# Optimization experiments

Measured on AMD Instinct MI355X. Metric: run time of the kernel, lower is better.

Reference implementation:

```python
import jax, jax.numpy as jnp
import numpy as np

B, L, D, H = 2, 2048, 2048, 16
Dh = D // H
THETA = 10000.0
NEG = -1e9


def _rope_tables(length, offset=0):
    # inv_freq: [Dh/2], positions: [L]
    inv_freq = 1.0 / (THETA ** (jnp.arange(0, Dh, 2, dtype=jnp.float32) / Dh))
    pos = jnp.arange(offset, offset + length, dtype=jnp.float32)
    freqs = pos[:, None] * inv_freq[None, :]           # [L, Dh/2]
    emb = jnp.concatenate([freqs, freqs], axis=-1)     # [L, Dh]
    return jnp.cos(emb), jnp.sin(emb)


def _rotate_half(t):
    t1, t2 = t[..., : Dh // 2], t[..., Dh // 2:]
    return jnp.concatenate([-t2, t1], axis=-1)


def setup_inputs() -> dict:
    key = jax.random.key(0)
    k1, k2, k3 = jax.random.split(key, 3)
    x = jax.random.normal(k1, (B, L, D), dtype=jnp.float32)
    attention_mask = jnp.ones((B, L), dtype=jnp.int32)
    w_qkv = jax.random.normal(k2, (D, 3 * D), dtype=jnp.float32) * (D ** -0.5)
    w_proj = jax.random.normal(k3, (D, D), dtype=jnp.float32) * (D ** -0.5)
    return {"x": x, "attention_mask": attention_mask, "w_qkv": w_qkv, "w_proj": w_proj}


def reference(x, attention_mask, w_qkv, w_proj):
    # QKV projection (no bias)
    qkv = x @ w_qkv                                    # [B, L, 3D]
    q, k, v = jnp.split(qkv, 3, axis=-1)
    q = q.reshape(B, L, H, Dh).transpose(0, 2, 1, 3)   # [B, H, L, Dh]
    k = k.reshape(B, L, H, Dh).transpose(0, 2, 1, 3)
    v = v.reshape(B, L, H, Dh).transpose(0, 2, 1, 3)

    # RoPE (past_len = 0)
    cos, sin = _rope_tables(L)                         # [L, Dh]
    q = q * cos + _rotate_half(q) * sin
    k = k * cos + _rotate_half(k) * sin

    # causal + key-padding mask (True = masked out)
    causal = jnp.triu(jnp.ones((L, L), dtype=bool), k=1)         # [L, L]
    pad = (attention_mask == 0)[:, None, None, :]                # [B,1,1,L]
    mask = causal[None, None, :, :] | pad                        # [B,1,L,L]

    scale = Dh ** -0.5
    scores = jnp.einsum("bhqd,bhkd->bhqk", q, k) * scale         # [B,H,L,L]
    scores = jnp.where(mask, NEG, scores)
    attn = jax.nn.softmax(scores, axis=-1)
    y = jnp.einsum("bhqk,bhkd->bhqd", attn, v)                   # [B,H,L,Dh]
    y = y.transpose(0, 2, 1, 3).reshape(B, L, D)
    return y @ w_proj
```

## Files before the change

### kernel.cpp

```cpp
#include <hip/hip_runtime.h>
#include <hip/hip_bf16.h>

typedef unsigned short ushort_t;
typedef __attribute__((ext_vector_type(4))) float fvec4;
typedef __attribute__((ext_vector_type(16))) float fvec16;
typedef __attribute__((ext_vector_type(8))) short short8;
typedef __attribute__((ext_vector_type(4))) unsigned short usvec4;
typedef __attribute__((ext_vector_type(2))) unsigned int uvec2;

typedef const __attribute__((address_space(1))) void* gas_ptr;
typedef __attribute__((address_space(3))) void* las_ptr;

__device__ __forceinline__ void glds16(const void* g, void* l) {
  __builtin_amdgcn_global_load_lds((gas_ptr)g, (las_ptr)l, 16, 0, 0);
}

__device__ __forceinline__ ushort_t f2bf(float f) {
  unsigned u = __float_as_uint(f);
  u += 0x7FFFu + ((u >> 16) & 1u);
  return (ushort_t)(u >> 16);
}
__device__ __forceinline__ float bf2f(ushort_t h) {
  return __uint_as_float(((unsigned)h) << 16);
}

__device__ __forceinline__ void swap32(unsigned& a, unsigned& b) {
#if __has_builtin(__builtin_amdgcn_permlane32_swap)
  uvec2 r = __builtin_amdgcn_permlane32_swap(a, b, false, false);
  a = r[0]; b = r[1];
#else
  const unsigned sa = (unsigned)__shfl_xor((int)a, 32);
  const unsigned sb = (unsigned)__shfl_xor((int)b, 32);
  const bool hi = (threadIdx.x & 32) != 0;
  const unsigned na = hi ? sb : a;
  const unsigned nb = hi ? b : sa;
  a = na; b = nb;
#endif
}

__global__ __launch_bounds__(256) void cast_f32_bf16(const float* __restrict__ X,
                                                     ushort_t* __restrict__ Xb) {
  const size_t i = ((size_t)blockIdx.x * 256 + threadIdx.x) * 4;
  const fvec4 v = *(const fvec4*)(X + i);
  usvec4 o;
  o[0] = f2bf(v[0]); o[1] = f2bf(v[1]); o[2] = f2bf(v[2]); o[3] = f2bf(v[3]);
  *(usvec4*)(Xb + i) = o;
}

__global__ __launch_bounds__(256) void tcast(const float* __restrict__ W,
                                             ushort_t* __restrict__ Wt,
                                             const int Kd, const int Nd) {
  __shared__ float ls[64][65];
  const int t = threadIdx.x;
  const int n0 = blockIdx.x * 64, k0 = blockIdx.y * 64;
  const int kr = t >> 4, nc = (t & 15) * 4;
#pragma unroll
  for (int it = 0; it < 4; ++it) {
    const fvec4 v = *(const fvec4*)(W + (size_t)(k0 + it * 16 + kr) * Nd + n0 + nc);
    ls[it * 16 + kr][nc + 0] = v[0];
    ls[it * 16 + kr][nc + 1] = v[1];
    ls[it * 16 + kr][nc + 2] = v[2];
    ls[it * 16 + kr][nc + 3] = v[3];
  }
  __syncthreads();
  const int nr = t >> 2, kg = (t & 3) * 16;
  __align__(16) ushort_t tmp[16];
#pragma unroll
  for (int i = 0; i < 16; ++i) tmp[i] = f2bf(ls[kg + i][nr]);
  ushort_t* dst = Wt + (size_t)(n0 + nr) * Kd + k0 + kg;
  *(short8*)(dst)     = *(const short8*)(tmp);
  *(short8*)(dst + 8) = *(const short8*)(tmp + 8);
}

#define FENCE asm volatile("" ::: "memory")

__device__ __forceinline__ void stage_one(const ushort_t* __restrict__ G, const int grow,
                                          const int K, const int tk, ushort_t* ldsmat,
                                          const int lrow0, const int wv, const int lane) {
  const int rr = lane >> 3;
  const int kk = ((lane & 7) ^ rr) * 8;
  glds16(G + (size_t)(grow + wv * 8 + rr) * K + tk + kk,
         ldsmat + (lrow0 + wv * 8) * 64);
}

__device__ __forceinline__ short8 frag_ld(const ushort_t* ldsmat, const int rbase,
                                          const int kc, const int quad, const int mm) {
  const int r = rbase + mm;
  const int blk = r >> 6;
  const int pblk = ((blk & 1) << 1) | (blk >> 1);
  const int ldsrow = pblk * 64 + (r & 63);
  const int kb = (kc * 64 + quad * 16) ^ ((mm & 7) << 4);
  return *(const short8*)(ldsmat + ldsrow * 64 + (kb >> 1));
}

__device__ __forceinline__ short8 fragld128(const ushort_t* mat, const int row,
                                            const int kc, const int quad) {
  const int kb = (kc * 64 + quad * 16) ^ ((row & 7) << 4);
  return *(const short8*)(mat + row * 64 + (kb >> 1));
}

#define G192_LDA(Am, q_)                                                      \
  short8 af[2][2];                                                            \
  af[0][0] = frag_ld(Am, wr * 128 + (q_) * 32,      0, quad, mm);             \
  af[0][1] = frag_ld(Am, wr * 128 + (q_) * 32,      1, quad, mm);             \
  af[1][0] = frag_ld(Am, wr * 128 + (q_) * 32 + 16, 0, quad, mm);             \
  af[1][1] = frag_ld(Am, wr * 128 + (q_) * 32 + 16, 1, quad, mm);

#define G192_LDB(Bm)                                                          \
  _Pragma("unroll")                                                           \
  for (int j = 0; j < 3; ++j) {                                               \
    bfr[j][0] = fragld128(Bm, wc * 48 + j * 16 + mm, 0, quad);                \
    bfr[j][1] = fragld128(Bm, wc * 48 + j * 16 + mm, 1, quad);                \
  }

#define G192_MFMA(q_)                                                         \
  __builtin_amdgcn_s_setprio(1);                                              \
  _Pragma("unroll")                                                           \
  for (int ii = 0; ii < 2; ++ii)                                              \
  _Pragma("unroll")                                                           \
  for (int j = 0; j < 3; ++j) {                                               \
    acc[(q_) * 2 + ii][j] = __builtin_amdgcn_mfma_f32_16x16x32_bf16(          \
        af[ii][0], bfr[j][0], acc[(q_) * 2 + ii][j], 0, 0, 0);                \
    acc[(q_) * 2 + ii][j] = __builtin_amdgcn_mfma_f32_16x16x32_bf16(          \
        af[ii][1], bfr[j][1], acc[(q_) * 2 + ii][j], 0, 0, 0);                \
  }                                                                           \
  __builtin_amdgcn_s_setprio(0);

__global__ __launch_bounds__(512, 2) void gemm192(
    const ushort_t* __restrict__ A, const ushort_t* __restrict__ Bt,
    const int M, const int N, const int K, const int mode,
    float* __restrict__ C,
    ushort_t* __restrict__ Qo, ushort_t* __restrict__ Ko, ushort_t* __restrict__ Vo) {
  __shared__ __align__(16) ushort_t lds[2][28672];

  const int tid = threadIdx.x, wv = tid >> 6, lane = tid & 63;
  const int quad = lane >> 4, mm = lane & 15;
  const int wr = wv >> 2, wc = wv & 3;

  const int nwg = gridDim.x, ntx = N / 192;
  const int bid = blockIdx.x;
  const int swz = (bid & 7) * (nwg >> 3) + (bid >> 3);
  const int by = swz / ntx, bx = swz - by * ntx;
  const int row0 = by * 256, col0 = bx * 192;

  fvec4 acc[8][3];
#pragma unroll
  for (int i = 0; i < 8; ++i)
#pragma unroll
    for (int j = 0; j < 3; ++j) acc[i][j] = (fvec4){0.f, 0.f, 0.f, 0.f};

  short8 bfr[3][2];

  ushort_t* A0 = &lds[0][0];      ushort_t* B0 = &lds[0][16384];
  ushort_t* A1 = &lds[1][0];      ushort_t* B1 = &lds[1][16384];

  stage_one(Bt, col0 + 0,   K, 0,  B0, 0,   wv, lane); FENCE;
  stage_one(Bt, col0 + 64,  K, 0,  B0, 64,  wv, lane); FENCE;
  stage_one(Bt, col0 + 128, K, 0,  B0, 128, wv, lane); FENCE;
  stage_one(A,  row0 + 0,   K, 0,  A0, 0,   wv, lane); FENCE;
  stage_one(A,  row0 + 64,  K, 0,  A0, 128, wv, lane); FENCE;
  stage_one(A,  row0 + 128, K, 0,  A0, 64,  wv, lane); FENCE;
  stage_one(A,  row0 + 192, K, 0,  A0, 192, wv, lane); FENCE;
  stage_one(Bt, col0 + 0,   K, 64, B1, 0,   wv, lane); FENCE;
  stage_one(Bt, col0 + 64,  K, 64, B1, 64,  wv, lane); FENCE;
  stage_one(Bt, col0 + 128, K, 64, B1, 128, wv, lane); FENCE;
  stage_one(A,  row0 + 0,   K, 64, A1, 0,   wv, lane); FENCE;
  stage_one(A,  row0 + 128, K, 64, A1, 64,  wv, lane); FENCE;
  asm volatile("s_waitcnt vmcnt(5)" ::: "memory");
  __builtin_amdgcn_s_barrier();

  const int nit = K >> 7;
  for (int i = 0; i < nit; ++i) {
    const bool more = (i + 1 < nit);
    const int kA = i * 128 + 64;
    const int kB = i * 128 + 128;
    const int kC = i * 128 + 192;
    {
      __builtin_amdgcn_s_barrier();
      G192_LDA(A0, 0);
      G192_LDB(B0);
      stage_one(A, row0 + 64,  K, kA, A1, 128, wv, lane); FENCE;
      stage_one(A, row0 + 192, K, kA, A1, 192, wv, lane);
      G192_MFMA(0);
    }
    {
      __builtin_amdgcn_s_barrier();
      G192_LDA(A0, 1);
      if (more) { stage_one(Bt, col0 + 0,  K, kB, B0, 0,  wv, lane); FENCE;
                  stage_one(Bt, col0 + 64, K, kB, B0, 64, wv, lane); }
      G192_MFMA(1);
    }
    {
      __builtin_amdgcn_s_barrier();
      G192_LDA(A0, 2);
      if (more) stage_one(Bt, col0 + 128, K, kB, B0, 128, wv, lane);
      G192_MFMA(2);
    }
    {
      __builtin_amdgcn_s_barrier();
      G192_LDA(A0, 3);
      if (more) {
        stage_one(A, row0 + 0,   K, kB, A0, 0,  wv, lane); FENCE;
        stage_one(A, row0 + 128, K, kB, A0, 64, wv, lane);
        asm volatile("s_waitcnt vmcnt(5)" ::: "memory");
      } else {
        asm volatile("s_waitcnt vmcnt(0)" ::: "memory");
      }
      G192_MFMA(3);
    }
    {
      __builtin_amdgcn_s_barrier();
      G192_LDA(A1, 0);
      G192_LDB(B1);
      if (more) { stage_one(A, row0 + 64,  K, kB, A0, 128, wv, lane); FENCE;
                  stage_one(A, row0 + 192, K, kB, A0, 192, wv, lane); }
      G192_MFMA(0);
    }
    {
      __builtin_amdgcn_s_barrier();
      G192_LDA(A1, 1);
      if (more) { stage_one(Bt, col0 + 0,  K, kC, B1, 0,  wv, lane); FENCE;
                  stage_one(Bt, col0 + 64, K, kC, B1, 64, wv, lane); }
      G192_MFMA(1);
    }
    {
      __builtin_amdgcn_s_barrier();
      G192_LDA(A1, 2);
      if (more) stage_one(Bt, col0 + 128, K, kC, B1, 128, wv, lane);
      G192_MFMA(2);
    }
    {
      __builtin_amdgcn_s_barrier();
      G192_LDA(A1, 3);
      if (more) {
        stage_one(A, row0 + 0,   K, kC, A1, 0,  wv, lane); FENCE;
        stage_one(A, row0 + 128, K, kC, A1, 64, wv, lane);
        asm volatile("s_waitcnt vmcnt(5)" ::: "memory");
      }
      G192_MFMA(3);
    }
  }

  if (mode == 0) {
#pragma unroll
    for (int i = 0; i < 8; ++i)
#pragma unroll
      for (int r = 0; r < 4; ++r) {
        const int row = row0 + wr * 128 + i * 16 + quad * 4 + r;
        float* cr = C + (size_t)row * N + col0 + wc * 48;
#pragma unroll
        for (int j = 0; j < 3; ++j) cr[j * 16 + mm] = acc[i][j][r];
      }
  } else {
#pragma unroll
    for (int j = 0; j < 3; ++j) {
      const int gcolj = col0 + wc * 48 + j * 16;
      const int which = gcolj >> 11;
      const int h = (gcolj >> 7) & 15;
      const int coff = (gcolj & 127) + mm;
      ushort_t* dst = (which == 0) ? Qo : (which == 1) ? Ko : Vo;
#pragma unroll
      for (int i = 0; i < 8; ++i)
#pragma unroll
        for (int r = 0; r < 4; ++r) {
          const int row = row0 + wr * 128 + i * 16 + quad * 4 + r;
          const int bb = row >> 11, l = row & 2047;
          dst[((size_t)(bb * 16 + h) * 2048 + l) * 128 + coff] = f2bf(acc[i][j][r]);
        }
    }
  }
}

__device__ __forceinline__ void stage_a128(const ushort_t* __restrict__ G, const int row0,
                                           const int K, const int tk, ushort_t* ldsA,
                                           const int wv, const int lane) {
  const int rr = lane >> 3;
  const int kk = ((lane & 7) ^ rr) * 8;
  const int r = wv * 8 + rr;
  glds16(G + (size_t)(row0 + r) * K + tk + kk,      ldsA + (wv * 8) * 64);
  glds16(G + (size_t)(row0 + 64 + r) * K + tk + kk, ldsA + (64 + wv * 8) * 64);
}
__device__ __forceinline__ void stage_b128(const ushort_t* __restrict__ G, const int col0,
                                           const int K, const int tk, ushort_t* ldsB,
                                           const int u, const int wv, const int lane) {
  const int rr = lane >> 3;
  const int kk = ((lane & 7) ^ rr) * 8;
  const int r = u * 64 + wv * 8 + rr;
  glds16(G + (size_t)(col0 + r) * K + tk + kk,       ldsB + (u * 64 + wv * 8) * 64);
  glds16(G + (size_t)(col0 + 128 + r) * K + tk + kk, ldsB + (128 + u * 64 + wv * 8) * 64);
}

__global__ __launch_bounds__(512, 2) void gemm128(
    const ushort_t* __restrict__ A, const ushort_t* __restrict__ Bt,
    const int M, const int N, const int K, const int mode,
    float* __restrict__ C,
    ushort_t* __restrict__ Qo, ushort_t* __restrict__ Ko, ushort_t* __restrict__ Vo) {
  __shared__ __align__(16) ushort_t l128[2][24576];

  const int tid = threadIdx.x, wv = tid >> 6, lane = tid & 63;
  const int quad = lane >> 4, mm = lane & 15;
  const int wr = wv >> 2, wc = wv & 3;

  const int nwg = gridDim.x, ntx = N >> 8;
  const int bid = blockIdx.x;
  const int swz = (bid & 7) * (nwg >> 3) + (bid >> 3);
  const int by = swz / ntx, bx = swz - by * ntx;
  const int row0 = by * 128, col0 = bx * 256;

  fvec4 acc[4][4];
#pragma unroll
  for (int m = 0; m < 4; ++m)
#pragma unroll
    for (int j = 0; j < 4; ++j) acc[m][j] = (fvec4){0.f, 0.f, 0.f, 0.f};

  ushort_t* A0 = &l128[0][0];     ushort_t* B0 = &l128[0][8192];
  ushort_t* A1 = &l128[1][0];     ushort_t* B1 = &l128[1][8192];

  short8 bfr[4][2];

  stage_b128(Bt, col0, K, 0,  B0, 0, wv, lane); FENCE;
  stage_b128(Bt, col0, K, 0,  B0, 1, wv, lane); FENCE;
  stage_a128(A,  row0, K, 0,  A0,    wv, lane); FENCE;
  stage_b128(Bt, col0, K, 64, B1, 0, wv, lane); FENCE;
  stage_b128(Bt, col0, K, 64, B1, 1, wv, lane); FENCE;
  asm volatile("s_waitcnt vmcnt(4)" ::: "memory");
  __builtin_amdgcn_s_barrier();

  const int nit = K >> 7;
  for (int i = 0; i < nit; ++i) {
    const bool more = (i + 1 < nit);
    const int kA = i * 128 + 64;
    const int kB = i * 128 + 128;
    const int kC = i * 128 + 192;
    {
      stage_a128(A, row0, K, kA, A1, wv, lane);
      short8 af[4];
#pragma unroll
      for (int m = 0; m < 4; ++m) af[m] = fragld128(A0, wr * 64 + m * 16 + mm, 0, quad);
#pragma unroll
      for (int j = 0; j < 4; ++j) {
        bfr[j][0] = fragld128(B0, wc * 64 + j * 16 + mm, 0, quad);
        bfr[j][1] = fragld128(B0, wc * 64 + j * 16 + mm, 1, quad);
      }
      __builtin_amdgcn_s_setprio(1);
#pragma unroll
      for (int m = 0; m < 4; ++m)
#pragma unroll
        for (int j = 0; j < 4; ++j)
          acc[m][j] = __builtin_amdgcn_mfma_f32_16x16x32_bf16(af[m], bfr[j][0], acc[m][j], 0, 0, 0);
      __builtin_amdgcn_s_setprio(0);
      asm volatile("s_waitcnt lgkmcnt(0)" ::: "memory");
      __builtin_amdgcn_sched_barrier(0);
    }
    {
      __builtin_amdgcn_s_barrier();
      if (more) { stage_b128(Bt, col0, K, kB, B0, 0, wv, lane); FENCE;
                  stage_b128(Bt, col0, K, kB, B0, 1, wv, lane); FENCE; }
      if (more) { asm volatile("s_waitcnt vmcnt(4)" ::: "memory"); }
      else      { asm volatile("s_waitcnt vmcnt(0)" ::: "memory"); }
      short8 af[4];
#pragma unroll
      for (int m = 0; m < 4; ++m) af[m] = fragld128(A0, wr * 64 + m * 16 + mm, 1, quad);
      __builtin_amdgcn_s_setprio(1);
#pragma unroll
      for (int m = 0; m < 4; ++m)
#pragma unroll
        for (int j = 0; j < 4; ++j)
          acc[m][j] = __builtin_amdgcn_mfma_f32_16x16x32_bf16(af[m], bfr[j][1], acc[m][j], 0, 0, 0);
      __builtin_amdgcn_s_setprio(0);
    }
    {
      __builtin_amdgcn_s_barrier();
      if (more) stage_a128(A, row0, K, kB, A0, wv, lane);
      short8 af[4];
#pragma unroll
      for (int m = 0; m < 4; ++m) af[m] = fragld128(A1, wr * 64 + m * 16 + mm, 0, quad);
#pragma unroll
      for (int j = 0; j < 4; ++j) {
        bfr[j][0] = fragld128(B1, wc * 64 + j * 16 + mm, 0, quad);
        bfr[j][1] = fragld128(B1, wc * 64 + j * 16 + mm, 1, quad);
      }
      __builtin_amdgcn_s_setprio(1);
#pragma unroll
      for (int m = 0; m < 4; ++m)
#pragma unroll
        for (int j = 0; j < 4; ++j)
          acc[m][j] = __builtin_amdgcn_mfma_f32_16x16x32_bf16(af[m], bfr[j][0], acc[m][j], 0, 0, 0);
      __builtin_amdgcn_s_setprio(0);
      asm volatile("s_waitcnt lgkmcnt(0)" ::: "memory");
      __builtin_amdgcn_sched_barrier(0);
    }
    {
      __builtin_amdgcn_s_barrier();
      if (more) { stage_b128(Bt, col0, K, kC, B1, 0, wv, lane); FENCE;
                  stage_b128(Bt, col0, K, kC, B1, 1, wv, lane); FENCE;
                  asm volatile("s_waitcnt vmcnt(4)" ::: "memory"); }
      short8 af[4];
#pragma unroll
      for (int m = 0; m < 4; ++m) af[m] = fragld128(A1, wr * 64 + m * 16 + mm, 1, quad);
      __builtin_amdgcn_s_setprio(1);
#pragma unroll
      for (int m = 0; m < 4; ++m)
#pragma unroll
        for (int j = 0; j < 4; ++j)
          acc[m][j] = __builtin_amdgcn_mfma_f32_16x16x32_bf16(af[m], bfr[j][1], acc[m][j], 0, 0, 0);
      __builtin_amdgcn_s_setprio(0);
      __builtin_amdgcn_s_barrier();
    }
  }

  if (mode == 0) {
#pragma unroll
    for (int m = 0; m < 4; ++m)
#pragma unroll
      for (int r = 0; r < 4; ++r) {
        const int row = row0 + wr * 64 + m * 16 + quad * 4 + r;
        float* cr = C + (size_t)row * N + col0 + wc * 64;
#pragma unroll
        for (int j = 0; j < 4; ++j) cr[j * 16 + mm] = acc[m][j][r];
      }
  } else {
    const int gcol = col0 + wc * 64;
    const int which = gcol >> 11;
    const int h = (gcol >> 7) & 15;
    const int coff = gcol & 127;
    ushort_t* dst = (which == 0) ? Qo : (which == 1) ? Ko : Vo;
#pragma unroll
    for (int m = 0; m < 4; ++m)
#pragma unroll
      for (int r = 0; r < 4; ++r) {
        const int row = row0 + wr * 64 + m * 16 + quad * 4 + r;
        const int bb = row >> 11, l = row & 2047;
        ushort_t* dr = dst + ((size_t)(bb * 16 + h) * 2048 + l) * 128 + coff;
#pragma unroll
        for (int j = 0; j < 4; ++j) dr[j * 16 + mm] = f2bf(acc[m][j][r]);
      }
  }
}

__global__ __launch_bounds__(256) void rope_kernel(ushort_t* Qb, ushort_t* Kb) {
  const int gid = blockIdx.x * 256 + threadIdx.x;
  const int pd = gid & 63;
  const int row = gid >> 6;
  const int l = row & 2047;
  ushort_t* base = (blockIdx.y ? Kb : Qb) + (size_t)row * 128;
  const float a = bf2f(base[pd]);
  const float bv = bf2f(base[pd + 64]);
  const float invf_rev = exp2f(-(float)pd * 0.20762050593045702f) * 0.15915494309189535f;
  float rev = (float)l * invf_rev;
  rev -= floorf(rev);
  const float ang = rev * 6.283185307179586f;
  float s, c;
  __sincosf(ang, &s, &c);
  float na = a * c - bv * s;
  float nb = bv * c + a * s;
  if (blockIdx.y == 0) { na *= 0.08838834764831845f; nb *= 0.08838834764831845f; }
  base[pd] = f2bf(na);
  base[pd + 64] = f2bf(nb);
}

__global__ __launch_bounds__(256) void vtrans_kernel(const ushort_t* __restrict__ Vn,
                                                     ushort_t* __restrict__ Vt) {
  __shared__ ushort_t ls[128 * 132];
  const int bh = blockIdx.x >> 4;
  const int l0 = (blockIdx.x & 15) * 128;
  const int t = threadIdx.x;
  const ushort_t* src = Vn + ((size_t)bh * 2048 + l0) * 128;
#pragma unroll
  for (int it = 0; it < 16; ++it) {
    const int c = it * 256 + t;
    const int lr = c >> 5, dc = (c & 31) * 4;
    *(usvec4*)(ls + lr * 132 + dc) = *(const usvec4*)(src + lr * 128 + dc);
  }
  __syncthreads();
  ushort_t* dstb = Vt + (size_t)bh * 128 * 2048 + l0;
#pragma unroll
  for (int it = 0; it < 16; ++it) {
    const int c = it * 256 + t;
    const int d = c >> 5, lc = (c & 31) * 4;
    usvec4 o;
    o[0] = ls[(lc + 0) * 132 + d];
    o[1] = ls[(lc + 1) * 132 + d];
    o[2] = ls[(lc + 2) * 132 + d];
    o[3] = ls[(lc + 3) * 132 + d];
    *(usvec4*)(dstb + (size_t)d * 2048 + lc) = o;
  }
}

__global__ __launch_bounds__(256, 2) void flash_kernel(
    const ushort_t* __restrict__ Qb, const ushort_t* __restrict__ Kb,
    const ushort_t* __restrict__ Vt, const int* __restrict__ am,
    ushort_t* __restrict__ Y) {
  __shared__ __align__(16) ushort_t lK[2][8192];
  __shared__ __align__(16) ushort_t lV[2][8192];
  __shared__ float lds_l[128];

  const int tid = threadIdx.x, wv = tid >> 6, lane = tid & 63;
  const int lh = lane >> 5, cq = lane & 31;
  const int bid = blockIdx.x;
  const int bh = bid & 31;
  const int qi = 15 - (bid >> 5);
  const int b = bh >> 4, head = bh & 15;
  const size_t qkBase = (size_t)bh * (2048 * 128);
  const int qb = qi * 128 + wv * 32;
  const int q = qb + cq;

  unsigned fullbits = 0;
  {
    const int* amr = am + b * 2048;
#pragma unroll
    for (int rgn = 0; rgn < 4; ++rgn) {
      const int4 a0 = *(const int4*)(amr + rgn * 512 + lane * 8);
      const int4 a1 = *(const int4*)(amr + rgn * 512 + lane * 8 + 4);
      const bool ok8 = a0.x && a0.y && a0.z && a0.w && a1.x && a1.y && a1.z && a1.w;
      const unsigned long long bal = __ballot(ok8);
#pragma unroll
      for (int tt = 0; tt < 8; ++tt)
        fullbits |= ((((bal >> (8 * tt)) & 0xFFull) == 0xFFull) ? 1u : 0u) << (rgn * 8 + tt);
    }
  }

  short8 qf[8];
  {
    const ushort_t* qrow = Qb + qkBase + (size_t)q * 128;
#pragma unroll
    for (int c = 0; c < 8; ++c) qf[c] = *(const short8*)(qrow + c * 16 + lh * 8);
  }

  fvec16 yacc[4];
#pragma unroll
  for (int i = 0; i < 4; ++i)
#pragma unroll
    for (int r = 0; r < 16; ++r) yacc[i][r] = 0.f;
  float psum = 0.f;

#define FLASH_STAGE(dK, dV, kk0)                                                          \
  _Pragma("unroll")                                                                       \
  for (int it = 0; it < 4; ++it) {                                                        \
    const int f_ = it * 4 + wv;                                                           \
    const int ct_ = f_ >> 3, c_ = f_ & 7;                                                 \
    glds16(Kb + qkBase + (size_t)((kk0) + ct_ * 32 + cq) * 128 + c_ * 16 + lh * 8,        \
           (dK) + f_ * 512);                                                              \
    const int dt_ = f_ >> 2, kc_ = f_ & 3;                                                \
    glds16(Vt + ((size_t)bh * 128 + dt_ * 32 + cq) * 2048 + (kk0) + kc_ * 16 + lh * 8,    \
           (dV) + f_ * 512);                                                              \
  }

  const int nt = qi * 2 + 2;
  FLASH_STAGE(&lK[0][0], &lV[0][0], 0)
  __syncthreads();

  int cur = 0;
  for (int t = 0; t < nt; ++t) {
    const int k0 = t * 64;
    if (t + 1 < nt) {
      FLASH_STAGE(&lK[cur ^ 1][0], &lV[cur ^ 1][0], k0 + 64)
    }

    if (k0 <= qb + 31) {
      const ushort_t* bK = &lK[cur][0];
      const ushort_t* bV = &lV[cur][0];
      const bool maskfull = (fullbits >> t) & 1u;
      unsigned long long keymask = ~0ull;
      if (!maskfull) keymask = __ballot(am[b * 2048 + k0 + lane] != 0);
      const bool fullvalid = (k0 + 63 <= qb) && maskfull;

#pragma unroll
      for (int ct = 0; ct < 2; ++ct) {
        fvec16 sA_, sB_;
#pragma unroll
        for (int r = 0; r < 16; ++r) { sA_[r] = 0.f; sB_[r] = 0.f; }
        __builtin_amdgcn_s_setprio(1);
#pragma unroll
        for (int c = 0; c < 4; ++c) {
          short8 kf = *(const short8*)(bK + (ct * 8 + c) * 512 + lane * 8);
          sA_ = __builtin_amdgcn_mfma_f32_32x32x16_bf16(kf, qf[c], sA_, 0, 0, 0);
        }
#pragma unroll
        for (int c = 4; c < 8; ++c) {
          short8 kf = *(const short8*)(bK + (ct * 8 + c) * 512 + lane * 8);
          sB_ = __builtin_amdgcn_mfma_f32_32x32x16_bf16(kf, qf[c], sB_, 0, 0, 0);
        }
        __builtin_amdgcn_s_setprio(0);
        float p[16];
        if (fullvalid) {
#pragma unroll
          for (int r = 0; r < 16; ++r) p[r] = __expf(sA_[r] + sB_[r]);
        } else {
#pragma unroll
          for (int r = 0; r < 16; ++r) {
            const int kl = (r & 3) + 8 * (r >> 2) + 4 * lh + ct * 32;
            const bool ok = (k0 + kl <= q) && (((keymask >> kl) & 1ull) != 0);
            p[r] = ok ? __expf(sA_[r] + sB_[r]) : 0.f;
          }
        }
#pragma unroll
        for (int r = 0; r < 16; ++r) psum += p[r];
        unsigned pk[8];
#pragma unroll
        for (int j = 0; j < 8; ++j) {
          __hip_bfloat162 t2 = __float22bfloat162_rn(make_float2(p[2 * j], p[2 * j + 1]));
          pk[j] = *(unsigned*)&t2;
        }
#pragma unroll
        for (int kc2 = 0; kc2 < 2; ++kc2) {
          unsigned a0 = pk[kc2 * 4 + 0], a2 = pk[kc2 * 4 + 2];
          unsigned a1 = pk[kc2 * 4 + 1], a3 = pk[kc2 * 4 + 3];
          swap32(a0, a2);
          swap32(a1, a3);
          union { unsigned u[4]; short8 s; } pf;
          pf.u[0] = a0; pf.u[1] = a1; pf.u[2] = a2; pf.u[3] = a3;
          const int kc = ct * 2 + kc2;
          __builtin_amdgcn_s_setprio(1);
#pragma unroll
          for (int dt = 0; dt < 4; ++dt) {
            short8 vf = *(const short8*)(bV + (dt * 4 + kc) * 512 + lane * 8);
            yacc[dt] = __builtin_amdgcn_mfma_f32_32x32x16_bf16(pf.s, vf, yacc[dt], 0, 0, 0);
          }
          __builtin_amdgcn_s_setprio(0);
        }
      }
    }
    __syncthreads();
    cur ^= 1;
  }
#undef FLASH_STAGE

  psum += __shfl_xor(psum, 32);
  if (lane < 32) lds_l[wv * 32 + lane] = psum;
  float inv16[16];
#pragma unroll
  for (int r = 0; r < 16; ++r)
    inv16[r] = 1.f / lds_l[wv * 32 + (r & 3) + 8 * (r >> 2) + 4 * lh];

#pragma unroll
  for (int dt = 0; dt < 4; ++dt)
#pragma unroll
    for (int r = 0; r < 16; ++r) {
      const int qloc = (r & 3) + 8 * (r >> 2) + 4 * lh;
      ushort_t* dst = Y + ((size_t)(b * 2048 + qb + qloc)) * 2048 + head * 128 + dt * 32 + cq;
      *dst = f2bf(yacc[dt][r] * inv16[r]);
    }
}

extern "C" void kernel_launch(void* const* d_in, const int* in_sizes, int n_in,
                              void* d_out, int out_size, void* d_ws, size_t ws_size,
                              hipStream_t stream) {
  const float* x      = (const float*)d_in[0];
  const int*   amask  = (const int*)d_in[1];
  const float* w_qkv  = (const float*)d_in[2];
  const float* w_proj = (const float*)d_in[3];

  ushort_t* xb     = (ushort_t*)d_ws;
  ushort_t* wqkvT  = xb + 8388608;
  ushort_t* wprojT = wqkvT + 12582912;
  ushort_t* Qb     = wprojT + 4194304;
  ushort_t* Kb     = Qb + 8388608;
  ushort_t* Vn     = Kb + 8388608;
  ushort_t* Vt     = wqkvT;
  ushort_t* Yb     = xb;

  cast_f32_bf16<<<8192, 256, 0, stream>>>(x, xb);
  tcast<<<dim3(96, 32), 256, 0, stream>>>(w_qkv, wqkvT, 2048, 6144);
  tcast<<<dim3(32, 32), 256, 0, stream>>>(w_proj, wprojT, 2048, 2048);
  gemm192<<<512, 512, 0, stream>>>(xb, wqkvT, 4096, 6144, 2048, 1,
                                   nullptr, Qb, Kb, Vn);
  rope_kernel<<<dim3(16384, 2), 256, 0, stream>>>(Qb, Kb);
  vtrans_kernel<<<512, 256, 0, stream>>>(Vn, Vt);
  flash_kernel<<<512, 256, 0, stream>>>(Qb, Kb, Vt, amask, Yb);
  gemm128<<<256, 512, 0, stream>>>(Yb, wprojT, 4096, 2048, 2048, 0,
                                   (float*)d_out, nullptr, nullptr, nullptr);
}
```

Measured before the change: 383.1 us.

## Shrink QKV GEMM tile to 128x192 with 4 waves/SIMD occupancy and new pipeline

Replaces the 256x192 QKV projection GEMM tile with a 128x192 tile, halving LDS use and accumulator registers. Launch bounds are raised to allow four blocks per CU, and the grid doubles to 1024 blocks. The pipeline is restructured into four phases per 128-K step with explicit lgkmcnt waits and sched barriers. This trades per-block data reuse for higher occupancy and better load balance over the CUs.

```diff
diff --git a/kernel.cpp b/kernel.cpp
--- a/kernel.cpp
+++ b/kernel.cpp
@@ -83,55 +83,45 @@
          ldsmat + (lrow0 + wv * 8) * 64);
 }
 
-__device__ __forceinline__ short8 frag_ld(const ushort_t* ldsmat, const int rbase,
-                                          const int kc, const int quad, const int mm) {
-  const int r = rbase + mm;
-  const int blk = r >> 6;
-  const int pblk = ((blk & 1) << 1) | (blk >> 1);
-  const int ldsrow = pblk * 64 + (r & 63);
-  const int kb = (kc * 64 + quad * 16) ^ ((mm & 7) << 4);
-  return *(const short8*)(ldsmat + ldsrow * 64 + (kb >> 1));
-}
-
 __device__ __forceinline__ short8 fragld128(const ushort_t* mat, const int row,
                                             const int kc, const int quad) {
   const int kb = (kc * 64 + quad * 16) ^ ((row & 7) << 4);
   return *(const short8*)(mat + row * 64 + (kb >> 1));
 }
 
-#define G192_LDA(Am, q_)                                                      \
+#define GQ_LDA(Am, g_)                                                        \
   short8 af[2][2];                                                            \
-  af[0][0] = frag_ld(Am, wr * 128 + (q_) * 32,      0, quad, mm);             \
-  af[0][1] = frag_ld(Am, wr * 128 + (q_) * 32,      1, quad, mm);             \
-  af[1][0] = frag_ld(Am, wr * 128 + (q_) * 32 + 16, 0, quad, mm);             \
-  af[1][1] = frag_ld(Am, wr * 128 + (q_) * 32 + 16, 1, quad, mm);
-
-#define G192_LDB(Bm)                                                          \
+  af[0][0] = fragld128(Am, wr * 64 + (g_) * 32 + mm,      0, quad);           \
+  af[0][1] = fragld128(Am, wr * 64 + (g_) * 32 + mm,      1, quad);           \
+  af[1][0] = fragld128(Am, wr * 64 + (g_) * 32 + 16 + mm, 0, quad);           \
+  af[1][1] = fragld128(Am, wr * 64 + (g_) * 32 + 16 + mm, 1, quad);
+
+#define GQ_LDB(Bm)                                                            \
   _Pragma("unroll")                                                           \
   for (int j = 0; j < 3; ++j) {                                               \
     bfr[j][0] = fragld128(Bm, wc * 48 + j * 16 + mm, 0, quad);                \
     bfr[j][1] = fragld128(Bm, wc * 48 + j * 16 + mm, 1, quad);                \
   }
 
-#define G192_MFMA(q_)                                                         \
+#define GQ_MFMA(g_)                                                           \
   __builtin_amdgcn_s_setprio(1);                                              \
   _Pragma("unroll")                                                           \
   for (int ii = 0; ii < 2; ++ii)                                              \
   _Pragma("unroll")                                                           \
   for (int j = 0; j < 3; ++j) {                                               \
-    acc[(q_) * 2 + ii][j] = __builtin_amdgcn_mfma_f32_16x16x32_bf16(          \
-        af[ii][0], bfr[j][0], acc[(q_) * 2 + ii][j], 0, 0, 0);                \
-    acc[(q_) * 2 + ii][j] = __builtin_amdgcn_mfma_f32_16x16x32_bf16(          \
-        af[ii][1], bfr[j][1], acc[(q_) * 2 + ii][j], 0, 0, 0);                \
+    acc[(g_) * 2 + ii][j] = __builtin_amdgcn_mfma_f32_16x16x32_bf16(          \
+        af[ii][0], bfr[j][0], acc[(g_) * 2 + ii][j], 0, 0, 0);                \
+    acc[(g_) * 2 + ii][j] = __builtin_amdgcn_mfma_f32_16x16x32_bf16(          \
+        af[ii][1], bfr[j][1], acc[(g_) * 2 + ii][j], 0, 0, 0);                \
   }                                                                           \
   __builtin_amdgcn_s_setprio(0);
 
-__global__ __launch_bounds__(512, 2) void gemm192(
+__global__ __launch_bounds__(512, 4) void gemmq(
     const ushort_t* __restrict__ A, const ushort_t* __restrict__ Bt,
     const int M, const int N, const int K, const int mode,
     float* __restrict__ C,
     ushort_t* __restrict__ Qo, ushort_t* __restrict__ Ko, ushort_t* __restrict__ Vo) {
-  __shared__ __align__(16) ushort_t lds[2][28672];
+  __shared__ __align__(16) ushort_t lds[2][20480];
 
   const int tid = threadIdx.x, wv = tid >> 6, lane = tid & 63;
   const int quad = lane >> 4, mm = lane & 15;
@@ -141,32 +131,28 @@
   const int bid = blockIdx.x;
   const int swz = (bid & 7) * (nwg >> 3) + (bid >> 3);
   const int by = swz / ntx, bx = swz - by * ntx;
-  const int row0 = by * 256, col0 = bx * 192;
-
-  fvec4 acc[8][3];
-#pragma unroll
-  for (int i = 0; i < 8; ++i)
+  const int row0 = by * 128, col0 = bx * 192;
+
+  fvec4 acc[4][3];
+#pragma unroll
+  for (int i = 0; i < 4; ++i)
 #pragma unroll
     for (int j = 0; j < 3; ++j) acc[i][j] = (fvec4){0.f, 0.f, 0.f, 0.f};
 
   short8 bfr[3][2];
 
-  ushort_t* A0 = &lds[0][0];      ushort_t* B0 = &lds[0][16384];
-  ushort_t* A1 = &lds[1][0];      ushort_t* B1 = &lds[1][16384];
+  ushort_t* A0 = &lds[0][0];      ushort_t* B0 = &lds[0][8192];
+  ushort_t* A1 = &lds[1][0];      ushort_t* B1 = &lds[1][8192];
 
   stage_one(Bt, col0 + 0,   K, 0,  B0, 0,   wv, lane); FENCE;
   stage_one(Bt, col0 + 64,  K, 0,  B0, 64,  wv, lane); FENCE;
   stage_one(Bt, col0 + 128, K, 0,  B0, 128, wv, lane); FENCE;
   stage_one(A,  row0 + 0,   K, 0,  A0, 0,   wv, lane); FENCE;
-  stage_one(A,  row0 + 64,  K, 0,  A0, 128, wv, lane); FENCE;
-  stage_one(A,  row0 + 128, K, 0,  A0, 64,  wv, lane); FENCE;
-  stage_one(A,  row0 + 192, K, 0,  A0, 192, wv, lane); FENCE;
+  stage_one(A,  row0 + 64,  K, 0,  A0, 64,  wv, lane); FENCE;
   stage_one(Bt, col0 + 0,   K, 64, B1, 0,   wv, lane); FENCE;
   stage_one(Bt, col0 + 64,  K, 64, B1, 64,  wv, lane); FENCE;
   stage_one(Bt, col0 + 128, K, 64, B1, 128, wv, lane); FENCE;
-  stage_one(A,  row0 + 0,   K, 64, A1, 0,   wv, lane); FENCE;
-  stage_one(A,  row0 + 128, K, 64, A1, 64,  wv, lane); FENCE;
-  asm volatile("s_waitcnt vmcnt(5)" ::: "memory");
+  asm volatile("s_waitcnt vmcnt(3)" ::: "memory");
   __builtin_amdgcn_s_barrier();
 
   const int nit = K >> 7;
@@ -176,80 +162,55 @@
     const int kB = i * 128 + 128;
     const int kC = i * 128 + 192;
     {
-      __builtin_amdgcn_s_barrier();
-      G192_LDA(A0, 0);
-      G192_LDB(B0);
-      stage_one(A, row0 + 64,  K, kA, A1, 128, wv, lane); FENCE;
-      stage_one(A, row0 + 192, K, kA, A1, 192, wv, lane);
-      G192_MFMA(0);
-    }
-    {
-      __builtin_amdgcn_s_barrier();
-      G192_LDA(A0, 1);
-      if (more) { stage_one(Bt, col0 + 0,  K, kB, B0, 0,  wv, lane); FENCE;
-                  stage_one(Bt, col0 + 64, K, kB, B0, 64, wv, lane); }
-      G192_MFMA(1);
-    }
-    {
-      __builtin_amdgcn_s_barrier();
-      G192_LDA(A0, 2);
-      if (more) stage_one(Bt, col0 + 128, K, kB, B0, 128, wv, lane);
-      G192_MFMA(2);
-    }
-    {
-      __builtin_amdgcn_s_barrier();
-      G192_LDA(A0, 3);
-      if (more) {
-        stage_one(A, row0 + 0,   K, kB, A0, 0,  wv, lane); FENCE;
-        stage_one(A, row0 + 128, K, kB, A0, 64, wv, lane);
-        asm volatile("s_waitcnt vmcnt(5)" ::: "memory");
-      } else {
-        asm volatile("s_waitcnt vmcnt(0)" ::: "memory");
-      }
-      G192_MFMA(3);
-    }
-    {
-      __builtin_amdgcn_s_barrier();
-      G192_LDA(A1, 0);
-      G192_LDB(B1);
-      if (more) { stage_one(A, row0 + 64,  K, kB, A0, 128, wv, lane); FENCE;
-                  stage_one(A, row0 + 192, K, kB, A0, 192, wv, lane); }
-      G192_MFMA(0);
-    }
-    {
-      __builtin_amdgcn_s_barrier();
-      G192_LDA(A1, 1);
-      if (more) { stage_one(Bt, col0 + 0,  K, kC, B1, 0,  wv, lane); FENCE;
-                  stage_one(Bt, col0 + 64, K, kC, B1, 64, wv, lane); }
-      G192_MFMA(1);
-    }
-    {
-      __builtin_amdgcn_s_barrier();
-      G192_LDA(A1, 2);
-      if (more) stage_one(Bt, col0 + 128, K, kC, B1, 128, wv, lane);
-      G192_MFMA(2);
-    }
-    {
-      __builtin_amdgcn_s_barrier();
-      G192_LDA(A1, 3);
-      if (more) {
-        stage_one(A, row0 + 0,   K, kC, A1, 0,  wv, lane); FENCE;
-        stage_one(A, row0 + 128, K, kC, A1, 64, wv, lane);
-        asm volatile("s_waitcnt vmcnt(5)" ::: "memory");
-      }
-      G192_MFMA(3);
+      stage_one(A, row0 + 0,  K, kA, A1, 0,  wv, lane); FENCE;
+      stage_one(A, row0 + 64, K, kA, A1, 64, wv, lane);
+      GQ_LDA(A0, 0);
+      GQ_LDB(B0);
+      GQ_MFMA(0);
+      asm volatile("s_waitcnt lgkmcnt(0)" ::: "memory");
+      __builtin_amdgcn_sched_barrier(0);
+    }
+    {
+      __builtin_amdgcn_s_barrier();
+      if (more) { stage_one(Bt, col0 + 0,   K, kB, B0, 0,   wv, lane); FENCE;
+                  stage_one(Bt, col0 + 64,  K, kB, B0, 64,  wv, lane); FENCE;
+                  stage_one(Bt, col0 + 128, K, kB, B0, 128, wv, lane); FENCE;
+                  asm volatile("s_waitcnt vmcnt(3)" ::: "memory"); }
+      else      { asm volatile("s_waitcnt vmcnt(0)" ::: "memory"); }
+      GQ_LDA(A0, 1);
+      GQ_MFMA(1);
+    }
+    {
+      __builtin_amdgcn_s_barrier();
+      if (more) { stage_one(A, row0 + 0,  K, kB, A0, 0,  wv, lane); FENCE;
+                  stage_one(A, row0 + 64, K, kB, A0, 64, wv, lane); }
+      GQ_LDA(A1, 0);
+      GQ_LDB(B1);
+      GQ_MFMA(0);
+      asm volatile("s_waitcnt lgkmcnt(0)" ::: "memory");
+      __builtin_amdgcn_sched_barrier(0);
+    }
+    {
+      __builtin_amdgcn_s_barrier();
+      if (more) { stage_one(Bt, col0 + 0,   K, kC, B1, 0,   wv, lane); FENCE;
+                  stage_one(Bt, col0 + 64,  K, kC, B1, 64,  wv, lane); FENCE;
+                  stage_one(Bt, col0 + 128, K, kC, B1, 128, wv, lane); FENCE;
+                  asm volatile("s_waitcnt vmcnt(3)" ::: "memory"); }
+      GQ_LDA(A1, 1);
+      GQ_MFMA(1);
+      __builtin_amdgcn_s_barrier();
     }
   }
 
   if (mode == 0) {
 #pragma unroll
-    for (int i = 0; i < 8; ++i)
+    for (int m = 0; m < 4; ++m)
 #pragma unroll
       for (int r = 0; r < 4; ++r) {
-        const int row = row0 + wr * 128 + i * 16 + quad * 4 + r;
+        const int row = row0 + wr * 64 + m * 16 + quad * 4 + r;
         float* cr = C + (size_t)row * N + col0 + wc * 48;
 #pragma unroll
-        for (int j = 0; j < 3; ++j) cr[j * 16 + mm] = acc[i][j][r];
+        for (int j = 0; j < 3; ++j) cr[j * 16 + mm] = acc[m][j][r];
       }
   } else {
 #pragma unroll
@@ -260,12 +221,12 @@
       const int coff = (gcolj & 127) + mm;
       ushort_t* dst = (which == 0) ? Qo : (which == 1) ? Ko : Vo;
 #pragma unroll
-      for (int i = 0; i < 8; ++i)
+      for (int m = 0; m < 4; ++m)
 #pragma unroll
         for (int r = 0; r < 4; ++r) {
-          const int row = row0 + wr * 128 + i * 16 + quad * 4 + r;
+          const int row = row0 + wr * 64 + m * 16 + quad * 4 + r;
           const int bb = row >> 11, l = row & 2047;
-          dst[((size_t)(bb * 16 + h) * 2048 + l) * 128 + coff] = f2bf(acc[i][j][r]);
+          dst[((size_t)(bb * 16 + h) * 2048 + l) * 128 + coff] = f2bf(acc[m][j][r]);
         }
     }
   }
@@ -663,8 +624,8 @@
   cast_f32_bf16<<<8192, 256, 0, stream>>>(x, xb);
   tcast<<<dim3(96, 32), 256, 0, stream>>>(w_qkv, wqkvT, 2048, 6144);
   tcast<<<dim3(32, 32), 256, 0, stream>>>(w_proj, wprojT, 2048, 2048);
-  gemm192<<<512, 512, 0, stream>>>(xb, wqkvT, 4096, 6144, 2048, 1,
-                                   nullptr, Qb, Kb, Vn);
+  gemmq<<<1024, 512, 0, stream>>>(xb, wqkvT, 4096, 6144, 2048, 1,
+                                  nullptr, Qb, Kb, Vn);
   rope_kernel<<<dim3(16384, 2), 256, 0, stream>>>(Qb, Kb);
   vtrans_kernel<<<512, 256, 0, stream>>>(Vn, Vt);
   flash_kernel<<<512, 256, 0, stream>>>(Qb, Kb, Vt, amask, Yb);
```

After: 411.4 us. 1.07x slower.

## Software-pipeline LDS fragment reads in QKV GEMM with double-buffered registers

Applied to the files above, without the earlier changes.

Reworks the QKV projection GEMM main loop so that the LDS fragment reads for the next sub-step are issued right after the current MFMA block, into alternating even/odd register buffers. This lets LDS latency overlap with MFMA work instead of stalling at the start of each sub-step. The vmcnt wait points are moved and retuned, and sched_barrier is added to hold the ordering. The cost is more live VGPRs under launch bounds (512, 2), and reading ahead across barriers depends on the staging order staying correct.

```diff
diff --git a/kernel.cpp b/kernel.cpp
--- a/kernel.cpp
+++ b/kernel.cpp
@@ -99,34 +99,34 @@
   return *(const short8*)(mat + row * 64 + (kb >> 1));
 }
 
-#define G192_LDA(Am, q_)                                                      \
-  short8 af[2][2];                                                            \
-  af[0][0] = frag_ld(Am, wr * 128 + (q_) * 32,      0, quad, mm);             \
-  af[0][1] = frag_ld(Am, wr * 128 + (q_) * 32,      1, quad, mm);             \
-  af[1][0] = frag_ld(Am, wr * 128 + (q_) * 32 + 16, 0, quad, mm);             \
-  af[1][1] = frag_ld(Am, wr * 128 + (q_) * 32 + 16, 1, quad, mm);
-
-#define G192_LDB(Bm)                                                          \
+#define G192_RD_A(dst_, Am, q_)                                               \
+  dst_[0][0] = frag_ld(Am, wr * 128 + (q_) * 32,      0, quad, mm);           \
+  dst_[0][1] = frag_ld(Am, wr * 128 + (q_) * 32,      1, quad, mm);           \
+  dst_[1][0] = frag_ld(Am, wr * 128 + (q_) * 32 + 16, 0, quad, mm);           \
+  dst_[1][1] = frag_ld(Am, wr * 128 + (q_) * 32 + 16, 1, quad, mm);
+
+#define G192_RD_B(dst_, Bm)                                                   \
   _Pragma("unroll")                                                           \
   for (int j = 0; j < 3; ++j) {                                               \
-    bfr[j][0] = fragld128(Bm, wc * 48 + j * 16 + mm, 0, quad);                \
-    bfr[j][1] = fragld128(Bm, wc * 48 + j * 16 + mm, 1, quad);                \
-  }
-
-#define G192_MFMA(q_)                                                         \
+    dst_[j][0] = fragld128(Bm, wc * 48 + j * 16 + mm, 0, quad);               \
+    dst_[j][1] = fragld128(Bm, wc * 48 + j * 16 + mm, 1, quad);               \
+  }
+
+#define G192_MFMA(af_, bf_, q_)                                               \
   __builtin_amdgcn_s_setprio(1);                                              \
   _Pragma("unroll")                                                           \
   for (int ii = 0; ii < 2; ++ii)                                              \
   _Pragma("unroll")                                                           \
   for (int j = 0; j < 3; ++j) {                                               \
     acc[(q_) * 2 + ii][j] = __builtin_amdgcn_mfma_f32_16x16x32_bf16(          \
-        af[ii][0], bfr[j][0], acc[(q_) * 2 + ii][j], 0, 0, 0);                \
+        af_[ii][0], bf_[j][0], acc[(q_) * 2 + ii][j], 0, 0, 0);               \
     acc[(q_) * 2 + ii][j] = __builtin_amdgcn_mfma_f32_16x16x32_bf16(          \
-        af[ii][1], bfr[j][1], acc[(q_) * 2 + ii][j], 0, 0, 0);                \
+        af_[ii][1], bf_[j][1], acc[(q_) * 2 + ii][j], 0, 0, 0);               \
   }                                                                           \
-  __builtin_amdgcn_s_setprio(0);
-
-__global__ __launch_bounds__(512, 2) void gemm192(
+  __builtin_amdgcn_s_setprio(0);                                              \
+  __builtin_amdgcn_sched_barrier(0);
+
+__global__ __launch_bounds__(512, 2) void gemm192p(
     const ushort_t* __restrict__ A, const ushort_t* __restrict__ Bt,
     const int M, const int N, const int K, const int mode,
     float* __restrict__ C,
@@ -149,7 +149,8 @@
 #pragma unroll
     for (int j = 0; j < 3; ++j) acc[i][j] = (fvec4){0.f, 0.f, 0.f, 0.f};
 
-  short8 bfr[3][2];
+  short8 bfrE[3][2], bfrO[3][2];
+  short8 afE[2][2], afO[2][2];
 
   ushort_t* A0 = &lds[0][0];      ushort_t* B0 = &lds[0][16384];
   ushort_t* A1 = &lds[1][0];      ushort_t* B1 = &lds[1][16384];
@@ -168,6 +169,8 @@
   stage_one(A,  row0 + 128, K, 64, A1, 64,  wv, lane); FENCE;
   asm volatile("s_waitcnt vmcnt(5)" ::: "memory");
   __builtin_amdgcn_s_barrier();
+  G192_RD_B(bfrE, B0);
+  G192_RD_A(afE, A0, 0);
 
   const int nit = K >> 7;
   for (int i = 0; i < nit; ++i) {
@@ -177,67 +180,61 @@
     const int kC = i * 128 + 192;
     {
       __builtin_amdgcn_s_barrier();
-      G192_LDA(A0, 0);
-      G192_LDB(B0);
       stage_one(A, row0 + 64,  K, kA, A1, 128, wv, lane); FENCE;
       stage_one(A, row0 + 192, K, kA, A1, 192, wv, lane);
-      G192_MFMA(0);
-    }
-    {
-      __builtin_amdgcn_s_barrier();
-      G192_LDA(A0, 1);
+      G192_MFMA(afE, bfrE, 0);
+      G192_RD_A(afO, A0, 1);
+    }
+    {
+      __builtin_amdgcn_s_barrier();
       if (more) { stage_one(Bt, col0 + 0,  K, kB, B0, 0,  wv, lane); FENCE;
                   stage_one(Bt, col0 + 64, K, kB, B0, 64, wv, lane); }
-      G192_MFMA(1);
-    }
-    {
-      __builtin_amdgcn_s_barrier();
-      G192_LDA(A0, 2);
-      if (more) stage_one(Bt, col0 + 128, K, kB, B0, 128, wv, lane);
-      G192_MFMA(2);
-    }
-    {
-      __builtin_amdgcn_s_barrier();
-      G192_LDA(A0, 3);
-      if (more) {
-        stage_one(A, row0 + 0,   K, kB, A0, 0,  wv, lane); FENCE;
-        stage_one(A, row0 + 128, K, kB, A0, 64, wv, lane);
-        asm volatile("s_waitcnt vmcnt(5)" ::: "memory");
-      } else {
-        asm volatile("s_waitcnt vmcnt(0)" ::: "memory");
-      }
-      G192_MFMA(3);
-    }
-    {
-      __builtin_amdgcn_s_barrier();
-      G192_LDA(A1, 0);
-      G192_LDB(B1);
+      G192_MFMA(afO, bfrE, 1);
+      G192_RD_A(afE, A0, 2);
+    }
+    {
+      __builtin_amdgcn_s_barrier();
+      if (more) { stage_one(Bt, col0 + 128, K, kB, B0, 128, wv, lane);
+                  asm volatile("s_waitcnt vmcnt(3)" ::: "memory");
+      } else {    asm volatile("s_waitcnt vmcnt(0)" ::: "memory"); }
+      G192_MFMA(afE, bfrE, 2);
+      G192_RD_A(afO, A0, 3);
+    }
+    {
+      __builtin_amdgcn_s_barrier();
+      if (more) { stage_one(A, row0 + 0,   K, kB, A0, 0,  wv, lane); FENCE;
+                  stage_one(A, row0 + 128, K, kB, A0, 64, wv, lane); }
+      G192_MFMA(afO, bfrE, 3);
+      G192_RD_B(bfrO, B1);
+      G192_RD_A(afE, A1, 0);
+    }
+    {
+      __builtin_amdgcn_s_barrier();
       if (more) { stage_one(A, row0 + 64,  K, kB, A0, 128, wv, lane); FENCE;
                   stage_one(A, row0 + 192, K, kB, A0, 192, wv, lane); }
-      G192_MFMA(0);
-    }
-    {
-      __builtin_amdgcn_s_barrier();
-      G192_LDA(A1, 1);
+      G192_MFMA(afE, bfrO, 0);
+      G192_RD_A(afO, A1, 1);
+    }
+    {
+      __builtin_amdgcn_s_barrier();
       if (more) { stage_one(Bt, col0 + 0,  K, kC, B1, 0,  wv, lane); FENCE;
                   stage_one(Bt, col0 + 64, K, kC, B1, 64, wv, lane); }
-      G192_MFMA(1);
-    }
-    {
-      __builtin_amdgcn_s_barrier();
-      G192_LDA(A1, 2);
-      if (more) stage_one(Bt, col0 + 128, K, kC, B1, 128, wv, lane);
-      G192_MFMA(2);
-    }
-    {
-      __builtin_amdgcn_s_barrier();
-      G192_LDA(A1, 3);
-      if (more) {
-        stage_one(A, row0 + 0,   K, kC, A1, 0,  wv, lane); FENCE;
-        stage_one(A, row0 + 128, K, kC, A1, 64, wv, lane);
-        asm volatile("s_waitcnt vmcnt(5)" ::: "memory");
-      }
-      G192_MFMA(3);
+      G192_MFMA(afO, bfrO, 1);
+      G192_RD_A(afE, A1, 2);
+    }
+    {
+      __builtin_amdgcn_s_barrier();
+      if (more) { stage_one(Bt, col0 + 128, K, kC, B1, 128, wv, lane);
+                  asm volatile("s_waitcnt vmcnt(3)" ::: "memory"); }
+      G192_MFMA(afE, bfrO, 2);
+      G192_RD_A(afO, A1, 3);
+    }
+    {
+      __builtin_amdgcn_s_barrier();
+      if (more) { stage_one(A, row0 + 0,   K, kC, A1, 0,  wv, lane); FENCE;
+                  stage_one(A, row0 + 128, K, kC, A1, 64, wv, lane); }
+      G192_MFMA(afO, bfrO, 3);
+      if (more) { G192_RD_B(bfrE, B0); G192_RD_A(afE, A0, 0); }
     }
   }
 
@@ -663,8 +660,8 @@
   cast_f32_bf16<<<8192, 256, 0, stream>>>(x, xb);
   tcast<<<dim3(96, 32), 256, 0, stream>>>(w_qkv, wqkvT, 2048, 6144);
   tcast<<<dim3(32, 32), 256, 0, stream>>>(w_proj, wprojT, 2048, 2048);
-  gemm192<<<512, 512, 0, stream>>>(xb, wqkvT, 4096, 6144, 2048, 1,
-                                   nullptr, Qb, Kb, Vn);
+  gemm192p<<<512, 512, 0, stream>>>(xb, wqkvT, 4096, 6144, 2048, 1,
+                                    nullptr, Qb, Kb, Vn);
   rope_kernel<<<dim3(16384, 2), 256, 0, stream>>>(Qb, Kb);
   vtrans_kernel<<<512, 256, 0, stream>>>(Vn, Vt);
   flash_kernel<<<512, 256, 0, stream>>>(Qb, Kb, Vt, amask, Yb);
```

After: 383.8 us. About the same (+0.2%).
